# Kernel tuning notes

Hardware: AMD Instinct MI355X
Metric: run time of the kernel (lower is better)

Reference implementation:

```python
import jax, jax.numpy as jnp
import numpy as np
from jax import lax

PS = 64          # patch_size
K = 256          # num_train_patches
COARSE = 4       # down_size_rate
TEMP = 0.1


def _avg_pool_stride(x, k):
    # avg_pool2d(x, kernel=k, stride=k); x: [B,1,H,W], H,W divisible by k
    B, C, H, W = x.shape
    return x.reshape(B, C, H // k, k, W // k, k).mean(axis=(3, 5))


def _avg_pool_s1(x, k):
    # avg_pool2d(x, kernel=k, stride=1, padding=VALID)
    s = lax.reduce_window(x, 0.0, lax.add, (1, 1, k, k), (1, 1, 1, 1), 'VALID')
    return s / float(k * k)


def _resize_bilinear(x, oh, ow):
    # F.interpolate mode='bilinear', align_corners=False; x: [B,1,H,W]
    B, C, H, W = x.shape

    def coords(n_in, n_out):
        c = (jnp.arange(n_out, dtype=jnp.float32) + 0.5) * (n_in / n_out) - 0.5
        c = jnp.clip(c, 0.0, n_in - 1)
        c0 = jnp.floor(c).astype(jnp.int32)
        c1 = jnp.minimum(c0 + 1, n_in - 1)
        return c0, c1, c - c0

    y0, y1, wy = coords(H, oh)
    x0, x1, wx = coords(W, ow)
    v00 = x[:, :, y0[:, None], x0[None, :]]
    v01 = x[:, :, y0[:, None], x1[None, :]]
    v10 = x[:, :, y1[:, None], x0[None, :]]
    v11 = x[:, :, y1[:, None], x1[None, :]]
    wy = wy[:, None]
    top = v00 * (1 - wx) + v01 * wx
    bot = v10 * (1 - wx) + v11 * wx
    return top * (1 - wy) + bot * wy


def _select_starts(coarse_pred, H, W, key):
    # coarse_pred: [B,1,H/COARSE,W/COARSE] -> sampled (h_starts, w_starts) [B,K]
    stride = max(1, PS // 8)
    coarse_kernel = max(1, PS // COARSE)
    fg = coarse_pred[:, 0:1]
    coarse_scores = _avg_pool_s1(fg, coarse_kernel)
    grid_h = (H - PS) // stride + 1
    grid_w = (W - PS) // stride + 1
    scores_map = _resize_bilinear(coarse_scores, grid_h, grid_w)
    flat = scores_map.reshape(scores_map.shape[0], -1)  # [B, grid_h*grid_w]
    smin = flat.min(axis=1, keepdims=True)
    smax = flat.max(axis=1, keepdims=True)
    rng = jnp.maximum(smax - smin, 1e-6)
    scaled = (flat - smin) / rng / TEMP  # logits of softmax probs
    # multinomial-without-replacement == Gumbel top-k on logits
    g = jax.random.gumbel(key, scaled.shape, dtype=scaled.dtype)
    _, top_idx = lax.top_k(scaled + g, K)  # [B,K]
    rows = top_idx // grid_w
    cols = top_idx % grid_w
    return rows * stride, cols * stride


def _gather_patches(img, h_starts, w_starts):
    # img: [B,C,H,W]; starts: [B,K] -> [B,K,C,PS,PS]
    C = img.shape[1]

    def one(im, h, w):  # im [C,H,W]
        return lax.dynamic_slice(im, (0, h, w), (C, PS, PS))

    return jax.vmap(jax.vmap(one, in_axes=(None, 0, 0)), in_axes=(0, 0, 0))(
        img, h_starts, w_starts)


def setup_inputs() -> dict:
    key = jax.random.key(0)
    k1, k2 = jax.random.split(key)
    image = jax.random.normal(k1, (8, 3, 1024, 1024), dtype=jnp.float32)
    labels = jax.random.uniform(k2, (8, 1, 1024, 1024), dtype=jnp.float32)
    return {"image": image, "labels": labels}


def reference(image, labels):
    B, C, H, W = image.shape
    coarse_pred = _avg_pool_stride(labels, COARSE)       # global branch (oracle)
    key = jax.random.key(42)
    h_starts, w_starts = _select_starts(coarse_pred, H, W, key)
    patches = _gather_patches(image, h_starts, w_starts)         # [B,K,C,PS,PS]
    label_patches = _gather_patches(labels, h_starts, w_starts)  # [B,K,1,PS,PS]
    coords = jnp.stack([h_starts, w_starts], axis=-1)            # [B,K,2]
    return patches, label_patches, coords
```

## Files before the change

kernel.cpp:

```cpp
#include <hip/hip_runtime.h>
#include <hip/hip_bf16.h>
#include <stdint.h>

#define B_     8
#define CSW    241
#define GW     121
#define NPB    14641
#define KSEL   256
#define TOTG   117128

#define NSEG   16
#define SEGLEN 916

#define PATCH_OFF   0
#define LABEL_OFF   25165824
#define COORD_OFF   33554432

#define FG_OFF    0
#define CS_OFF    524288
#define FLAT_OFF  988936
#define MM_OFF    1106064
#define KEY_OFF   1106080
#define CAND_OFF  1340336

__global__ void k_fg(const float* __restrict__ labels, float* __restrict__ fg) {
  int idx = blockIdx.x * 256 + threadIdx.x;
  int b = idx >> 16; int rem = idx & 65535;
  int oy = rem >> 8; int ox = rem & 255;
  const float* p = labels + (size_t)b * 1048576 + (size_t)oy * 4096 + ox * 4;
  float acc = 0.0f;
  #pragma unroll
  for (int dy = 0; dy < 4; ++dy) {
    const float* r = p + dy * 1024;
    #pragma unroll
    for (int dx = 0; dx < 4; ++dx) acc = __fadd_rn(acc, r[dx]);
  }
  fg[idx] = __fdiv_rn(acc, 16.0f);
}

__global__ void k_cs(const float* __restrict__ fg, float* __restrict__ cs) {
  int idx = blockIdx.x * 256 + threadIdx.x;
  if (idx >= B_ * CSW * CSW) return;
  int b = idx / (CSW * CSW); int rem = idx % (CSW * CSW);
  int oy = rem / CSW; int ox = rem % CSW;
  const float* p = fg + (size_t)b * 65536 + (size_t)oy * 256 + ox;
  float acc = 0.0f;
  for (int wy = 0; wy < 16; ++wy) {
    const float* r = p + wy * 256;
    #pragma unroll
    for (int wx = 0; wx < 16; ++wx) acc = __fadd_rn(acc, r[wx]);
  }
  cs[idx] = __fdiv_rn(acc, 256.0f);
}

__global__ void k_resize(const float* __restrict__ cs, float* __restrict__ flat) {
  int idx = blockIdx.x * 256 + threadIdx.x;
  if (idx >= B_ * NPB) return;
  int b = idx / NPB; int rem = idx % NPB;
  int oy = rem / GW; int ox = rem % GW;
  const float SCALE = (float)(241.0 / 121.0);

  float cy = __fsub_rn(__fmul_rn(__fadd_rn((float)oy, 0.5f), SCALE), 0.5f);
  cy = fminf(fmaxf(cy, 0.0f), 240.0f);
  int y0 = (int)floorf(cy); int y1 = min(y0 + 1, 240);
  float wy = __fsub_rn(cy, (float)y0);

  float cx = __fsub_rn(__fmul_rn(__fadd_rn((float)ox, 0.5f), SCALE), 0.5f);
  cx = fminf(fmaxf(cx, 0.0f), 240.0f);
  int x0 = (int)floorf(cx); int x1 = min(x0 + 1, 240);
  float wx = __fsub_rn(cx, (float)x0);

  const float* base = cs + (size_t)b * (CSW * CSW);
  float v00 = base[y0 * CSW + x0];
  float v01 = base[y0 * CSW + x1];
  float v10 = base[y1 * CSW + x0];
  float v11 = base[y1 * CSW + x1];
  float omwx = __fsub_rn(1.0f, wx), omwy = __fsub_rn(1.0f, wy);
  float top = __fadd_rn(__fmul_rn(v00, omwx), __fmul_rn(v01, wx));
  float bot = __fadd_rn(__fmul_rn(v10, omwx), __fmul_rn(v11, wx));
  flat[idx] = __fadd_rn(__fmul_rn(top, omwy), __fmul_rn(bot, wy));
}

__global__ void k_minmax(const float* __restrict__ flat, float* __restrict__ mm) {
  __shared__ float smn[256], smx[256];
  int b = blockIdx.x, tid = threadIdx.x;
  float mn = 3.402823466e38f, mx = -3.402823466e38f;
  for (int j = tid; j < NPB; j += 256) {
    float v = flat[(size_t)b * NPB + j];
    mn = fminf(mn, v); mx = fmaxf(mx, v);
  }
  smn[tid] = mn; smx[tid] = mx; __syncthreads();
  for (int s = 128; s > 0; s >>= 1) {
    if (tid < s) {
      smn[tid] = fminf(smn[tid], smn[tid + s]);
      smx[tid] = fmaxf(smx[tid], smx[tid + s]);
    }
    __syncthreads();
  }
  if (tid == 0) { mm[b] = smn[0]; mm[8 + b] = smx[0]; }
}

__device__ __forceinline__ void tf2(unsigned c0, unsigned c1,
                                    unsigned* o0, unsigned* o1) {
  const unsigned ks0 = 0u, ks1 = 42u, ks2 = 0x1BD11BDAu ^ 0u ^ 42u;
  unsigned x0 = c0 + ks0, x1 = c1 + ks1;
#define RND(r) { x0 += x1; x1 = (x1 << r) | (x1 >> (32 - r)); x1 ^= x0; }
  RND(13) RND(15) RND(26) RND(6)   x0 += ks1; x1 += ks2 + 1u;
  RND(17) RND(29) RND(16) RND(24)  x0 += ks2; x1 += ks0 + 2u;
  RND(13) RND(15) RND(26) RND(6)   x0 += ks0; x1 += ks1 + 3u;
  RND(17) RND(29) RND(16) RND(24)  x0 += ks1; x1 += ks2 + 4u;
  RND(13) RND(15) RND(26) RND(6)   x0 += ks2; x1 += ks0 + 5u;
#undef RND
  *o0 = x0; *o1 = x1;
}

__global__ void k_keys(const float* __restrict__ flat, const float* __restrict__ mm,
                       unsigned long long* __restrict__ keys) {
  int idx = blockIdx.x * 256 + threadIdx.x;
  if (idx >= TOTG) return;
  int b = idx / NPB; unsigned j = (unsigned)(idx % NPB);
  float smin = mm[b], smax = mm[8 + b];
  float rng = fmaxf(__fsub_rn(smax, smin), 1e-6f);
  float scaled = __fdiv_rn(__fdiv_rn(__fsub_rn(flat[idx], smin), rng), 0.1f);

  unsigned o0, o1;
  tf2(0u, (unsigned)idx, &o0, &o1);
  unsigned bits = o0 ^ o1;

  unsigned m = bits >> 9;
  float u = (m == 0u) ? 1.17549435e-38f
                      : __fsub_rn(__uint_as_float(0x3f800000u | m), 1.0f);
  float l1 = (float)::log((double)u);
  float a  = -l1;
  float l2 = (float)::log((double)a);
  float g  = -l2;

  float tot = __fadd_rn(scaled, g);
  unsigned s = __float_as_uint(tot);
  unsigned o = (s & 0x80000000u) ? ~s : (s | 0x80000000u);
  keys[idx] = ((unsigned long long)o << 32) | (unsigned long long)(j ^ 0xFFFFFFFFu);
}

__global__ void k_part(const unsigned long long* __restrict__ keys,
                       unsigned long long* __restrict__ cand) {
  __shared__ unsigned long long sm[1024];
  int blk = blockIdx.x;
  int b = blk >> 4, s = blk & 15;
  int base = s * SEGLEN;
  int len = min(SEGLEN, NPB - base);
  const unsigned long long* kb = keys + (size_t)b * NPB + base;
  int tid = threadIdx.x;
  for (int i = tid; i < 1024; i += 256) sm[i] = (i < len) ? kb[i] : 0ull;
  __syncthreads();

  for (int ksz = 2; ksz <= 1024; ksz <<= 1) {
    for (int j = ksz >> 1; j > 0; j >>= 1) {
      for (int i = tid; i < 1024; i += 256) {
        int ixj = i ^ j;
        if (ixj > i) {
          bool up = ((i & ksz) == 0);
          unsigned long long a = sm[i], c = sm[ixj];
          if ((a > c) == up) { sm[i] = c; sm[ixj] = a; }
        }
      }
      __syncthreads();
    }
  }
  cand[(size_t)blk * 256 + tid] = sm[1023 - tid];
}

__global__ void k_merge(const unsigned long long* __restrict__ cand,
                        float* __restrict__ coords) {
  __shared__ unsigned long long sm[4096];
  int b = blockIdx.x, tid = threadIdx.x;
  const unsigned long long* cb = cand + (size_t)b * 4096;
  for (int t = tid; t < 4096; t += 256) sm[t] = cb[t];
  __syncthreads();

  int g = 1;
  for (int m = NSEG; m > 1; m >>= 1, g <<= 1) {
    int half = m >> 1;
    for (int q = tid; q < half * 256; q += 256) {
      int p = q >> 8, i = q & 255;
      int A = (2 * p) * g * 256, Bb = (2 * p + 1) * g * 256;
      unsigned long long a = sm[A + i], c = sm[Bb + 255 - i];
      sm[A + i] = a > c ? a : c;
    }
    __syncthreads();
    for (int j = 128; j > 0; j >>= 1) {
      for (int q = tid; q < half * 128; q += 256) {
        int p = q >> 7, r = q & 127;
        int i = ((r & ~(j - 1)) << 1) | (r & (j - 1));
        int A = (2 * p) * g * 256;
        unsigned long long a = sm[A + i], c = sm[A + i + j];
        if (a < c) { sm[A + i] = c; sm[A + i + j] = a; }
      }
      __syncthreads();
    }
  }

  unsigned long long key = sm[tid];
  unsigned j = ((unsigned)(key & 0xFFFFFFFFull)) ^ 0xFFFFFFFFu;
  int row = j / GW, col = j % GW;
  coords[((size_t)b * KSEL + tid) * 2 + 0] = (float)(row * 8);
  coords[((size_t)b * KSEL + tid) * 2 + 1] = (float)(col * 8);
}

__global__ void k_gather(const float* __restrict__ image, const float* __restrict__ labels,
                         float* __restrict__ out) {
  int bk = blockIdx.x;
  int b = bk >> 8;
  const float* coords = out + COORD_OFF;
  int h = (int)coords[(size_t)bk * 2 + 0];
  int w = (int)coords[(size_t)bk * 2 + 1];

  const float* imgb = image + (size_t)b * 3145728;
  float* po = out + PATCH_OFF + (size_t)bk * 12288;
  for (int t = threadIdx.x; t < 12288; t += 256) {
    int c = t >> 12, rem = t & 4095, y = rem >> 6, x = rem & 63;
    po[t] = imgb[(size_t)c * 1048576 + (size_t)(h + y) * 1024 + (w + x)];
  }
  const float* labb = labels + (size_t)b * 1048576;
  float* lo = out + LABEL_OFF + (size_t)bk * 4096;
  for (int t = threadIdx.x; t < 4096; t += 256) {
    int y = t >> 6, x = t & 63;
    lo[t] = labb[(size_t)(h + y) * 1024 + (w + x)];
  }
}

extern "C" void kernel_launch(void* const* d_in, const int* in_sizes, int n_in,
                              void* d_out, int out_size, void* d_ws, size_t ws_size,
                              hipStream_t stream) {
  const float* image  = (const float*)d_in[0];
  const float* labels = (const float*)d_in[1];
  float* out = (float*)d_out;

  float* fg   = out + FG_OFF;
  float* cs   = out + CS_OFF;
  float* flat = out + FLAT_OFF;
  float* mm   = out + MM_OFF;
  unsigned long long* keys = (unsigned long long*)(out + KEY_OFF);
  unsigned long long* cand = (unsigned long long*)(out + CAND_OFF);
  float* coords = out + COORD_OFF;

  k_fg<<<2048, 256, 0, stream>>>(labels, fg);
  k_cs<<<(B_ * CSW * CSW + 255) / 256, 256, 0, stream>>>(fg, cs);
  k_resize<<<(TOTG + 255) / 256, 256, 0, stream>>>(cs, flat);
  k_minmax<<<B_, 256, 0, stream>>>(flat, mm);
  k_keys<<<(TOTG + 255) / 256, 256, 0, stream>>>(flat, mm, keys);
  k_part<<<B_ * NSEG, 256, 0, stream>>>(keys, cand);
  k_merge<<<B_, 256, 0, stream>>>(cand, coords);
  k_gather<<<2048, 256, 0, stream>>>(image, labels, out);
}
```

Baseline: 321.1 us.

## Fuse min/max into resize and key generation into partition sort, vectorize loads

```diff
diff --git a/kernel.cpp b/kernel.cpp
--- a/kernel.cpp
+++ b/kernel.cpp
@@ -4,6 +4,7 @@
 
 #define B_     8
 #define CSW    241
+#define CSG    61
 #define GW     121
 #define NPB    14641
 #define KSEL   256
@@ -20,84 +21,114 @@
 #define CS_OFF    524288
 #define FLAT_OFF  988936
 #define MM_OFF    1106064
-#define KEY_OFF   1106080
 #define CAND_OFF  1340336
+
+__device__ __forceinline__ unsigned enc_f(float f) {
+  unsigned s = __float_as_uint(f);
+  return (s & 0x80000000u) ? ~s : (s | 0x80000000u);
+}
+__device__ __forceinline__ float dec_f(unsigned o) {
+  unsigned s = (o & 0x80000000u) ? (o & 0x7FFFFFFFu) : ~o;
+  return __uint_as_float(s);
+}
 
 __global__ void k_fg(const float* __restrict__ labels, float* __restrict__ fg) {
   int idx = blockIdx.x * 256 + threadIdx.x;
   int b = idx >> 16; int rem = idx & 65535;
   int oy = rem >> 8; int ox = rem & 255;
-  const float* p = labels + (size_t)b * 1048576 + (size_t)oy * 4096 + ox * 4;
+  const float4* p = (const float4*)(labels + (size_t)b * 1048576 +
+                                    (size_t)oy * 4096 + ox * 4);
   float acc = 0.0f;
   #pragma unroll
   for (int dy = 0; dy < 4; ++dy) {
-    const float* r = p + dy * 1024;
-    #pragma unroll
-    for (int dx = 0; dx < 4; ++dx) acc = __fadd_rn(acc, r[dx]);
+    float4 v = p[dy * 256];
+    acc = __fadd_rn(acc, v.x); acc = __fadd_rn(acc, v.y);
+    acc = __fadd_rn(acc, v.z); acc = __fadd_rn(acc, v.w);
   }
   fg[idx] = __fdiv_rn(acc, 16.0f);
 }
 
-__global__ void k_cs(const float* __restrict__ fg, float* __restrict__ cs) {
+__global__ void k_cs(const float* __restrict__ fg, float* __restrict__ cs,
+                     unsigned* __restrict__ mm) {
+  if (blockIdx.x == 0 && threadIdx.x < 16)
+    mm[threadIdx.x] = (threadIdx.x < 8) ? 0xFFFFFFFFu : 0u;
+
   int idx = blockIdx.x * 256 + threadIdx.x;
-  if (idx >= B_ * CSW * CSW) return;
-  int b = idx / (CSW * CSW); int rem = idx % (CSW * CSW);
-  int oy = rem / CSW; int ox = rem % CSW;
-  const float* p = fg + (size_t)b * 65536 + (size_t)oy * 256 + ox;
-  float acc = 0.0f;
+  const int TOT = B_ * CSW * CSG;
+  if (idx >= TOT) return;
+  int b = idx / (CSW * CSG); int rem = idx % (CSW * CSG);
+  int oy = rem / CSG; int ox0 = (rem % CSG) * 4;
+  int nk = min(4, CSW - ox0);
+  int lv = nk + 15;
+  const float* p = fg + (size_t)b * 65536 + (size_t)oy * 256 + ox0;
+
+  float acc[4] = {0.0f, 0.0f, 0.0f, 0.0f};
   for (int wy = 0; wy < 16; ++wy) {
     const float* r = p + wy * 256;
+    float v[19];
     #pragma unroll
-    for (int wx = 0; wx < 16; ++wx) acc = __fadd_rn(acc, r[wx]);
-  }
-  cs[idx] = __fdiv_rn(acc, 256.0f);
-}
-
-__global__ void k_resize(const float* __restrict__ cs, float* __restrict__ flat) {
-  int idx = blockIdx.x * 256 + threadIdx.x;
-  if (idx >= B_ * NPB) return;
-  int b = idx / NPB; int rem = idx % NPB;
-  int oy = rem / GW; int ox = rem % GW;
-  const float SCALE = (float)(241.0 / 121.0);
-
-  float cy = __fsub_rn(__fmul_rn(__fadd_rn((float)oy, 0.5f), SCALE), 0.5f);
-  cy = fminf(fmaxf(cy, 0.0f), 240.0f);
-  int y0 = (int)floorf(cy); int y1 = min(y0 + 1, 240);
-  float wy = __fsub_rn(cy, (float)y0);
-
-  float cx = __fsub_rn(__fmul_rn(__fadd_rn((float)ox, 0.5f), SCALE), 0.5f);
-  cx = fminf(fmaxf(cx, 0.0f), 240.0f);
-  int x0 = (int)floorf(cx); int x1 = min(x0 + 1, 240);
-  float wx = __fsub_rn(cx, (float)x0);
-
-  const float* base = cs + (size_t)b * (CSW * CSW);
-  float v00 = base[y0 * CSW + x0];
-  float v01 = base[y0 * CSW + x1];
-  float v10 = base[y1 * CSW + x0];
-  float v11 = base[y1 * CSW + x1];
-  float omwx = __fsub_rn(1.0f, wx), omwy = __fsub_rn(1.0f, wy);
-  float top = __fadd_rn(__fmul_rn(v00, omwx), __fmul_rn(v01, wx));
-  float bot = __fadd_rn(__fmul_rn(v10, omwx), __fmul_rn(v11, wx));
-  flat[idx] = __fadd_rn(__fmul_rn(top, omwy), __fmul_rn(bot, wy));
-}
-
-__global__ void k_minmax(const float* __restrict__ flat, float* __restrict__ mm) {
-  __shared__ float smn[256], smx[256];
-  int b = blockIdx.x, tid = threadIdx.x;
-  float mn = 3.402823466e38f, mx = -3.402823466e38f;
-  for (int j = tid; j < NPB; j += 256) {
-    float v = flat[(size_t)b * NPB + j];
-    mn = fminf(mn, v); mx = fmaxf(mx, v);
+    for (int x = 0; x < 19; ++x) { v[x] = 0.0f; if (x < lv) v[x] = r[x]; }
+    #pragma unroll
+    for (int k = 0; k < 4; ++k) {
+      if (k < nk) {
+        #pragma unroll
+        for (int wx = 0; wx < 16; ++wx) acc[k] = __fadd_rn(acc[k], v[k + wx]);
+      }
+    }
+  }
+  float* co = cs + (size_t)b * (CSW * CSW) + (size_t)oy * CSW + ox0;
+  #pragma unroll
+  for (int k = 0; k < 4; ++k)
+    if (k < nk) co[k] = __fdiv_rn(acc[k], 256.0f);
+}
+
+__global__ void k_resize(const float* __restrict__ cs, float* __restrict__ flat,
+                         unsigned* __restrict__ mm) {
+  __shared__ unsigned smn[256], smx[256];
+  int b = blockIdx.y;
+  int rem = blockIdx.x * 256 + threadIdx.x;
+  int tid = threadIdx.x;
+  unsigned mn = 0xFFFFFFFFu, mx = 0u;
+
+  if (rem < NPB) {
+    int oy = rem / GW; int ox = rem % GW;
+    const float SCALE = (float)(241.0 / 121.0);
+
+    float cy = __fsub_rn(__fmul_rn(__fadd_rn((float)oy, 0.5f), SCALE), 0.5f);
+    cy = fminf(fmaxf(cy, 0.0f), 240.0f);
+    int y0 = (int)floorf(cy); int y1 = min(y0 + 1, 240);
+    float wy = __fsub_rn(cy, (float)y0);
+
+    float cx = __fsub_rn(__fmul_rn(__fadd_rn((float)ox, 0.5f), SCALE), 0.5f);
+    cx = fminf(fmaxf(cx, 0.0f), 240.0f);
+    int x0 = (int)floorf(cx); int x1 = min(x0 + 1, 240);
+    float wx = __fsub_rn(cx, (float)x0);
+
+    const float* base = cs + (size_t)b * (CSW * CSW);
+    float v00 = base[y0 * CSW + x0];
+    float v01 = base[y0 * CSW + x1];
+    float v10 = base[y1 * CSW + x0];
+    float v11 = base[y1 * CSW + x1];
+    float omwx = __fsub_rn(1.0f, wx), omwy = __fsub_rn(1.0f, wy);
+    float top = __fadd_rn(__fmul_rn(v00, omwx), __fmul_rn(v01, wx));
+    float bot = __fadd_rn(__fmul_rn(v10, omwx), __fmul_rn(v11, wx));
+    float val = __fadd_rn(__fmul_rn(top, omwy), __fmul_rn(bot, wy));
+    flat[(size_t)b * NPB + rem] = val;
+    unsigned o = enc_f(val);
+    mn = o; mx = o;
   }
   smn[tid] = mn; smx[tid] = mx; __syncthreads();
   for (int s = 128; s > 0; s >>= 1) {
     if (tid < s) {
-      smn[tid] = fminf(smn[tid], smn[tid + s]);
-      smx[tid] = fmaxf(smx[tid], smx[tid + s]);
+      smn[tid] = min(smn[tid], smn[tid + s]);
+      smx[tid] = max(smx[tid], smx[tid + s]);
     }
     __syncthreads();
   }
-  if (tid == 0) { mm[b] = smn[0]; mm[8 + b] = smx[0]; }
+  if (tid == 0) {
+    atomicMin(&mm[b], smn[0]);
+    atomicMax(&mm[8 + b], smx[0]);
+  }
 }
 
 __device__ __forceinline__ void tf2(unsigned c0, unsigned c1,
@@ -114,43 +145,43 @@
   *o0 = x0; *o1 = x1;
 }
 
-__global__ void k_keys(const float* __restrict__ flat, const float* __restrict__ mm,
-                       unsigned long long* __restrict__ keys) {
-  int idx = blockIdx.x * 256 + threadIdx.x;
-  if (idx >= TOTG) return;
-  int b = idx / NPB; unsigned j = (unsigned)(idx % NPB);
-  float smin = mm[b], smax = mm[8 + b];
-  float rng = fmaxf(__fsub_rn(smax, smin), 1e-6f);
-  float scaled = __fdiv_rn(__fdiv_rn(__fsub_rn(flat[idx], smin), rng), 0.1f);
-
-  unsigned o0, o1;
-  tf2(0u, (unsigned)idx, &o0, &o1);
-  unsigned bits = o0 ^ o1;
-
-  unsigned m = bits >> 9;
-  float u = (m == 0u) ? 1.17549435e-38f
-                      : __fsub_rn(__uint_as_float(0x3f800000u | m), 1.0f);
-  float l1 = (float)::log((double)u);
-  float a  = -l1;
-  float l2 = (float)::log((double)a);
-  float g  = -l2;
-
-  float tot = __fadd_rn(scaled, g);
-  unsigned s = __float_as_uint(tot);
-  unsigned o = (s & 0x80000000u) ? ~s : (s | 0x80000000u);
-  keys[idx] = ((unsigned long long)o << 32) | (unsigned long long)(j ^ 0xFFFFFFFFu);
-}
-
-__global__ void k_part(const unsigned long long* __restrict__ keys,
+__global__ void k_part(const float* __restrict__ flat, const unsigned* __restrict__ mm,
                        unsigned long long* __restrict__ cand) {
   __shared__ unsigned long long sm[1024];
   int blk = blockIdx.x;
   int b = blk >> 4, s = blk & 15;
   int base = s * SEGLEN;
   int len = min(SEGLEN, NPB - base);
-  const unsigned long long* kb = keys + (size_t)b * NPB + base;
   int tid = threadIdx.x;
-  for (int i = tid; i < 1024; i += 256) sm[i] = (i < len) ? kb[i] : 0ull;
+
+  float smin = dec_f(mm[b]), smax = dec_f(mm[8 + b]);
+  float rng = fmaxf(__fsub_rn(smax, smin), 1e-6f);
+
+  for (int i = tid; i < 1024; i += 256) {
+    unsigned long long kv = 0ull;
+    if (i < len) {
+      int j = base + i;
+      int idx = b * NPB + j;
+      float scaled = __fdiv_rn(__fdiv_rn(__fsub_rn(flat[idx], smin), rng), 0.1f);
+
+      unsigned o0, o1;
+      tf2(0u, (unsigned)idx, &o0, &o1);
+      unsigned bits = o0 ^ o1;
+
+      unsigned m = bits >> 9;
+      float u = (m == 0u) ? 1.17549435e-38f
+                          : __fsub_rn(__uint_as_float(0x3f800000u | m), 1.0f);
+      float l1 = (float)::log((double)u);
+      float a  = -l1;
+      float l2 = (float)::log((double)a);
+      float g  = -l2;
+
+      float tot = __fadd_rn(scaled, g);
+      unsigned o = enc_f(tot);
+      kv = ((unsigned long long)o << 32) | (unsigned long long)((unsigned)j ^ 0xFFFFFFFFu);
+    }
+    sm[i] = kv;
+  }
   __syncthreads();
 
   for (int ksz = 2; ksz <= 1024; ksz <<= 1) {
@@ -215,16 +246,17 @@
   int w = (int)coords[(size_t)bk * 2 + 1];
 
   const float* imgb = image + (size_t)b * 3145728;
-  float* po = out + PATCH_OFF + (size_t)bk * 12288;
-  for (int t = threadIdx.x; t < 12288; t += 256) {
-    int c = t >> 12, rem = t & 4095, y = rem >> 6, x = rem & 63;
-    po[t] = imgb[(size_t)c * 1048576 + (size_t)(h + y) * 1024 + (w + x)];
+  float4* po = (float4*)(out + PATCH_OFF + (size_t)bk * 12288);
+  for (int t = threadIdx.x; t < 3072; t += 256) {
+    int c = t >> 10, rem = t & 1023, y = rem >> 4, x4 = rem & 15;
+    po[t] = *(const float4*)(imgb + (size_t)c * 1048576 +
+                             (size_t)(h + y) * 1024 + w + x4 * 4);
   }
   const float* labb = labels + (size_t)b * 1048576;
-  float* lo = out + LABEL_OFF + (size_t)bk * 4096;
-  for (int t = threadIdx.x; t < 4096; t += 256) {
-    int y = t >> 6, x = t & 63;
-    lo[t] = labb[(size_t)(h + y) * 1024 + (w + x)];
+  float4* lo = (float4*)(out + LABEL_OFF + (size_t)bk * 4096);
+  for (int t = threadIdx.x; t < 1024; t += 256) {
+    int y = t >> 4, x4 = t & 15;
+    lo[t] = *(const float4*)(labb + (size_t)(h + y) * 1024 + w + x4 * 4);
   }
 }
 
@@ -238,17 +270,14 @@
   float* fg   = out + FG_OFF;
   float* cs   = out + CS_OFF;
   float* flat = out + FLAT_OFF;
-  float* mm   = out + MM_OFF;
-  unsigned long long* keys = (unsigned long long*)(out + KEY_OFF);
+  unsigned* mm = (unsigned*)(out + MM_OFF);
   unsigned long long* cand = (unsigned long long*)(out + CAND_OFF);
   float* coords = out + COORD_OFF;
 
   k_fg<<<2048, 256, 0, stream>>>(labels, fg);
-  k_cs<<<(B_ * CSW * CSW + 255) / 256, 256, 0, stream>>>(fg, cs);
-  k_resize<<<(TOTG + 255) / 256, 256, 0, stream>>>(cs, flat);
-  k_minmax<<<B_, 256, 0, stream>>>(flat, mm);
-  k_keys<<<(TOTG + 255) / 256, 256, 0, stream>>>(flat, mm, keys);
-  k_part<<<B_ * NSEG, 256, 0, stream>>>(keys, cand);
+  k_cs<<<(B_ * CSW * CSG + 255) / 256, 256, 0, stream>>>(fg, cs, mm);
+  k_resize<<<dim3((NPB + 255) / 256, B_), 256, 0, stream>>>(cs, flat, mm);
+  k_part<<<B_ * NSEG, 256, 0, stream>>>(flat, mm, cand);
   k_merge<<<B_, 256, 0, stream>>>(cand, coords);
   k_gather<<<2048, 256, 0, stream>>>(image, labels, out);
 }
```

Measured after the change: 309.9 us. 1.04x faster.
